# Kernel optimization log

Hardware: AMD Instinct MI355X
Metric: run time of the kernel (lower is better)

The kernel has to match this reference:

```python
import jax, jax.numpy as jnp
from jax import lax
import numpy as np

B, C, T = 16, 512, 4096
COEFF_INIT = 0.04


def setup_inputs() -> dict:
    key = jax.random.key(0)
    k1, k2 = jax.random.split(key)
    x = jax.random.normal(k1, (B, C, T), dtype=jnp.float32)
    # learned per-channel smoothing coefficients, initialized like the module
    weights = jnp.ones((C,), dtype=jnp.float32) * COEFF_INIT
    return {"x": x, "weights": weights}


def reference(x, weights):
    # clamp weights to [0, 1] (mirrors the in-place no-grad clamp; values stay
    # unchanged here since coeff_init is inside the range)
    s = jnp.clip(weights, 0.0, 1.0)  # [C]
    xt = jnp.moveaxis(x, 2, 0)       # [T, B, C]
    init = xt[0]                      # y_0 = x_0

    def step(acc, sample):
        acc = s * sample + (1.0 - s) * acc
        return acc, acc

    _, ys = lax.scan(step, init, xt[1:])          # [T-1, B, C]
    out = jnp.concatenate([init[None], ys], axis=0)  # [T, B, C]
    return jnp.moveaxis(out, 0, 2)                   # [B, C, T]
```

## Files before the change

### kernel.cpp

```cpp
#include <hip/hip_runtime.h>


constexpr int T_LEN = 4096;
constexpr int C_LEN = 512;
constexpr int BLOCK = 256;
constexpr int NW    = 4;
constexpr int CH    = 4;

typedef float nfloat4 __attribute__((ext_vector_type(4)));

__global__ __launch_bounds__(BLOCK) void ema_scan_kernel(
    const float* __restrict__ x,
    const float* __restrict__ w,
    float* __restrict__ y)
{
    const int row  = blockIdx.x;
    const int c    = row & (C_LEN - 1);
    const int tid  = threadIdx.x;
    const int lane = tid & 63;
    const int wv   = tid >> 6;

    float s = w[c];
    s = fminf(fmaxf(s, 0.0f), 1.0f);
    const float a = 1.0f - s;

    const nfloat4* xp = (const nfloat4*)(x + (size_t)row * T_LEN);
    nfloat4*       yp = (nfloat4*)(y + (size_t)row * T_LEN);

    nfloat4 v[CH];
    #pragma unroll
    for (int k = 0; k < CH; ++k)
        v[k] = xp[(k << 8) + (wv << 6) + lane];

    const float a2 = a * a, a3 = a2 * a, a4 = a2 * a2;

    float S[CH];
    #pragma unroll
    for (int k = 0; k < CH; ++k) {
        float l0 = s * v[k].x;
        if (k == 0 && tid == 0) l0 = v[0].x;
        float l1 = fmaf(a, l0, s * v[k].y);
        float l2 = fmaf(a, l1, s * v[k].z);
        float l3 = fmaf(a, l2, s * v[k].w);
        v[k].x = l0; v[k].y = l1; v[k].z = l2; v[k].w = l3;
        S[k] = l3;
    }

    float wgt = a4;
    #pragma unroll
    for (int d = 1; d < 64; d <<= 1) {
        #pragma unroll
        for (int k = 0; k < CH; ++k) {
            float up = __shfl_up(S[k], d, 64);
            if (lane >= d) S[k] = fmaf(wgt, up, S[k]);
        }
        wgt *= wgt;
    }
    const float a256 = wgt;

    __shared__ float tot[CH * NW];
    if (lane == 63) {
        #pragma unroll
        for (int k = 0; k < CH; ++k) tot[(k << 2) + wv] = S[k];
    }
    __syncthreads();

    float E[CH];
    {
        float R = 0.0f;
        #pragma unroll
        for (int m = 0; m < CH * NW; ++m) {
            if ((m & 3) == wv) E[m >> 2] = R;
            R = fmaf(a256, R, tot[m]);
        }
    }

    float powl = 1.0f, tq = a4;
    #pragma unroll
    for (int b = 0; b < 6; ++b) {
        if ((lane >> b) & 1) powl *= tq;
        tq *= tq;
    }

    #pragma unroll
    for (int k = 0; k < CH; ++k) {
        float Sx   = __shfl_up(S[k], 1, 64);
        float base = (lane == 0) ? 0.0f : Sx;
        float P    = fmaf(powl, E[k], base);
        nfloat4 o;
        o.x = fmaf(a,  P, v[k].x);
        o.y = fmaf(a2, P, v[k].y);
        o.z = fmaf(a3, P, v[k].z);
        o.w = fmaf(a4, P, v[k].w);
        __builtin_nontemporal_store(o, &yp[(k << 8) + (wv << 6) + lane]);
    }
}

extern "C" void kernel_launch(void* const* d_in, const int* in_sizes, int n_in,
                              void* d_out, int out_size, void* d_ws, size_t ws_size,
                              hipStream_t stream) {
    const float* x = (const float*)d_in[0];
    const float* w = (const float*)d_in[1];
    float* y = (float*)d_out;

    const int rows = out_size / T_LEN;
    ema_scan_kernel<<<rows, BLOCK, 0, stream>>>(x, w, y);
}
```

Measured before the change: 221.4 us.

## Make EMA scan kernel persistent with software-prefetched next row

Replaces the one-block-per-row launch with a fixed grid of 2048 blocks, each processing four rows in sequence. While the current row is scanned and stored, the block loads the next row into registers, so load latency overlaps with compute and stores. A double-buffered shared array avoids a second barrier per iteration. In exchange it uses more registers, which may lower occupancy, and it hardcodes the grid size so that it only covers B*C = 8192 rows.

```diff
diff --git a/kernel.cpp b/kernel.cpp
--- a/kernel.cpp
+++ b/kernel.cpp
@@ -6,93 +6,113 @@
 constexpr int BLOCK = 256;
 constexpr int NW    = 4;
 constexpr int CH    = 4;
+constexpr int GRID  = 2048;
+constexpr int GENS  = 4;
 
 typedef float nfloat4 __attribute__((ext_vector_type(4)));
 
-__global__ __launch_bounds__(BLOCK) void ema_scan_kernel(
+__global__ __launch_bounds__(BLOCK) void ema_persist_kernel(
     const float* __restrict__ x,
     const float* __restrict__ w,
     float* __restrict__ y)
 {
-    const int row  = blockIdx.x;
-    const int c    = row & (C_LEN - 1);
     const int tid  = threadIdx.x;
     const int lane = tid & 63;
     const int wv   = tid >> 6;
 
-    float s = w[c];
-    s = fminf(fmaxf(s, 0.0f), 1.0f);
-    const float a = 1.0f - s;
+    __shared__ float tot[2][CH * NW];
 
-    const nfloat4* xp = (const nfloat4*)(x + (size_t)row * T_LEN);
-    nfloat4*       yp = (nfloat4*)(y + (size_t)row * T_LEN);
-
-    nfloat4 v[CH];
-    #pragma unroll
-    for (int k = 0; k < CH; ++k)
-        v[k] = xp[(k << 8) + (wv << 6) + lane];
-
-    const float a2 = a * a, a3 = a2 * a, a4 = a2 * a2;
-
-    float S[CH];
-    #pragma unroll
-    for (int k = 0; k < CH; ++k) {
-        float l0 = s * v[k].x;
-        if (k == 0 && tid == 0) l0 = v[0].x;
-        float l1 = fmaf(a, l0, s * v[k].y);
-        float l2 = fmaf(a, l1, s * v[k].z);
-        float l3 = fmaf(a, l2, s * v[k].w);
-        v[k].x = l0; v[k].y = l1; v[k].z = l2; v[k].w = l3;
-        S[k] = l3;
-    }
-
-    float wgt = a4;
-    #pragma unroll
-    for (int d = 1; d < 64; d <<= 1) {
+    nfloat4 vc[CH];
+    {
+        const nfloat4* xp = (const nfloat4*)(x + (size_t)blockIdx.x * T_LEN);
         #pragma unroll
-        for (int k = 0; k < CH; ++k) {
-            float up = __shfl_up(S[k], d, 64);
-            if (lane >= d) S[k] = fmaf(wgt, up, S[k]);
-        }
-        wgt *= wgt;
-    }
-    const float a256 = wgt;
-
-    __shared__ float tot[CH * NW];
-    if (lane == 63) {
-        #pragma unroll
-        for (int k = 0; k < CH; ++k) tot[(k << 2) + wv] = S[k];
-    }
-    __syncthreads();
-
-    float E[CH];
-    {
-        float R = 0.0f;
-        #pragma unroll
-        for (int m = 0; m < CH * NW; ++m) {
-            if ((m & 3) == wv) E[m >> 2] = R;
-            R = fmaf(a256, R, tot[m]);
-        }
-    }
-
-    float powl = 1.0f, tq = a4;
-    #pragma unroll
-    for (int b = 0; b < 6; ++b) {
-        if ((lane >> b) & 1) powl *= tq;
-        tq *= tq;
+        for (int k = 0; k < CH; ++k)
+            vc[k] = xp[(k << 8) + (wv << 6) + lane];
     }
 
     #pragma unroll
-    for (int k = 0; k < CH; ++k) {
-        float Sx   = __shfl_up(S[k], 1, 64);
-        float base = (lane == 0) ? 0.0f : Sx;
-        float P    = fmaf(powl, E[k], base);
-        nfloat4 o;
-        o.x = fmaf(a,  P, v[k].x);
-        o.y = fmaf(a2, P, v[k].y);
-        o.z = fmaf(a3, P, v[k].z);
-        o.w = fmaf(a4, P, v[k].w);
-        __builtin_nontemporal_store(o, &yp[(k << 8) + (wv << 6) + lane]);
+    for (int g = 0; g < GENS; ++g) {
+        const int row = g * GRID + blockIdx.x;
+
+        nfloat4 vn[CH];
+        if (g < GENS - 1) {
+            const nfloat4* xn = (const nfloat4*)(x + (size_t)(row + GRID) * T_LEN);
+            #pragma unroll
+            for (int k = 0; k < CH; ++k)
+                vn[k] = xn[(k << 8) + (wv << 6) + lane];
+        }
+        __builtin_amdgcn_sched_barrier(0);
+
+        const int c = row & (C_LEN - 1);
+        float s = fminf(fmaxf(w[c], 0.0f), 1.0f);
+        const float a = 1.0f - s;
+        const float a2 = a * a, a3 = a2 * a, a4 = a2 * a2;
+
+        float S[CH];
+        #pragma unroll
+        for (int k = 0; k < CH; ++k) {
+            float l0 = s * vc[k].x;
+            if (k == 0 && tid == 0) l0 = vc[0].x;
+            float l1 = fmaf(a, l0, s * vc[k].y);
+            float l2 = fmaf(a, l1, s * vc[k].z);
+            float l3 = fmaf(a, l2, s * vc[k].w);
+            vc[k].x = l0; vc[k].y = l1; vc[k].z = l2; vc[k].w = l3;
+            S[k] = l3;
+        }
+
+        float wgt = a4;
+        #pragma unroll
+        for (int d = 1; d < 64; d <<= 1) {
+            #pragma unroll
+            for (int k = 0; k < CH; ++k) {
+                float up = __shfl_up(S[k], d, 64);
+                if (lane >= d) S[k] = fmaf(wgt, up, S[k]);
+            }
+            wgt *= wgt;
+        }
+        const float a256 = wgt;
+
+        if (lane == 63) {
+            #pragma unroll
+            for (int k = 0; k < CH; ++k) tot[g & 1][(k << 2) + wv] = S[k];
+        }
+        __syncthreads();
+
+        float E[CH];
+        {
+            float R = 0.0f;
+            #pragma unroll
+            for (int m = 0; m < CH * NW; ++m) {
+                if ((m & 3) == wv) E[m >> 2] = R;
+                R = fmaf(a256, R, tot[g & 1][m]);
+            }
+        }
+
+        float powl = 1.0f, tq = a4;
+        #pragma unroll
+        for (int b = 0; b < 6; ++b) {
+            if ((lane >> b) & 1) powl *= tq;
+            tq *= tq;
+        }
+
+        nfloat4* yp = (nfloat4*)(y + (size_t)row * T_LEN);
+        #pragma unroll
+        for (int k = 0; k < CH; ++k) {
+            float Sx   = __shfl_up(S[k], 1, 64);
+            float base = (lane == 0) ? 0.0f : Sx;
+            float P    = fmaf(powl, E[k], base);
+            nfloat4 o;
+            o.x = fmaf(a,  P, vc[k].x);
+            o.y = fmaf(a2, P, vc[k].y);
+            o.z = fmaf(a3, P, vc[k].z);
+            o.w = fmaf(a4, P, vc[k].w);
+            __builtin_nontemporal_store(o, &yp[(k << 8) + (wv << 6) + lane]);
+        }
+
+        if (g < GENS - 1) {
+            #pragma unroll
+            for (int k = 0; k < CH; ++k) vc[k] = vn[k];
+        }
     }
 }
 
@@ -103,6 +123,5 @@
     const float* w = (const float*)d_in[1];
     float* y = (float*)d_out;
 
-    const int rows = out_size / T_LEN;
-    ema_scan_kernel<<<rows, BLOCK, 0, stream>>>(x, w, y);
+    ema_persist_kernel<<<GRID, BLOCK, 0, stream>>>(x, w, y);
 }
```

Result: slower. 232.8 us (+5.2%).
